# Performance work log

Measured on AMD Instinct MI355X. Metric: run time of the kernel, lower is better.

## Reference

```python
import jax, jax.numpy as jnp
import numpy as np


def setup_inputs() -> dict:
    key = jax.random.key(0)
    ks = jax.random.split(key, 7)
    B, N, D, A = 32, 128, 512, 512
    sD = 1.0 / np.sqrt(D)
    sA = 1.0 / np.sqrt(A)
    return {
        "x": jax.random.normal(ks[0], (B, N, D), dtype=jnp.float32),
        "W1": jax.random.normal(ks[1], (A, D), dtype=jnp.float32) * sD,
        "b1": jax.random.normal(ks[2], (A,), dtype=jnp.float32) * sD,
        "W2": jax.random.normal(ks[3], (A, D), dtype=jnp.float32) * sD,
        "b2": jax.random.normal(ks[4], (A,), dtype=jnp.float32) * sD,
        "Wout": jax.random.normal(ks[5], (A,), dtype=jnp.float32) * sA,
        "bout": jax.random.normal(ks[6], (1,), dtype=jnp.float32) * sA,
    }


def reference(x, W1, b1, W2, b2, Wout, bout):
    # x: (B, N, D)
    x1 = jnp.einsum('bnd,ad->bna', x, W1) + b1  # mlp1 -> (B, N, A)
    x2 = jnp.einsum('bnd,ad->bna', x, W2) + b2  # mlp2 -> (B, N, A)
    # outer broadcast add: x1.unsqueeze(1) + x2.unsqueeze(2) -> (B, N, N, A)
    s = x1[:, None, :, :] + x2[:, :, None, :]
    # include_root=False: drop ROOT row along dim 1 -> (B, N-1, N, A)
    s = s[:, 1:, :, :]
    s = jnp.tanh(s)
    # out linear A -> 1, then squeeze -> (B, N-1, N)
    return jnp.einsum('bija,a->bij', s, Wout) + bout[0]
```

## Files before the change

kernel.cpp:

```cpp
#include <hip/hip_runtime.h>
#include <hip/hip_bf16.h>

#define B_ 32
#define N_ 128
#define D_ 512
#define A_ 512
#define R_ (B_*N_)
#define OC 1024
#define CEXP 2.8853900817779268f

typedef __attribute__((ext_vector_type(8)))  short frag_ab;
typedef __attribute__((ext_vector_type(16))) float frag_c;

__device__ inline unsigned pack2bf(float a, float b) {
    unsigned ua = __builtin_bit_cast(unsigned, a) + 0x8000u;
    unsigned ub = __builtin_bit_cast(unsigned, b) + 0x8000u;
    return __builtin_amdgcn_perm(ub, ua, 0x07060302);
}
__device__ inline float bf2f_lo(unsigned u){ return __builtin_bit_cast(float, u << 16); }
__device__ inline float bf2f_hi(unsigned u){ return __builtin_bit_cast(float, u & 0xffff0000u); }
__device__ inline void wr8(float* dst, uint4 v) {
    *(float4*)dst     = float4{bf2f_lo(v.x),bf2f_hi(v.x),bf2f_lo(v.y),bf2f_hi(v.y)};
    *(float4*)(dst+4) = float4{bf2f_lo(v.z),bf2f_hi(v.z),bf2f_lo(v.w),bf2f_hi(v.w)};
}

__global__ __launch_bounds__(256) void k0_cvt(
    const float* __restrict__ X, const float* __restrict__ W1,
    const float* __restrict__ W2,
    unsigned short* __restrict__ Xb, unsigned short* __restrict__ W1b,
    unsigned short* __restrict__ W2b)
{
    const int NX = R_*D_/8, NW = A_*D_/8;
    int i = blockIdx.x*256 + threadIdx.x;
    const float* src; unsigned short* dst; int off;
    if (i < NX)            { src = X;  dst = Xb;  off = i; }
    else if (i < NX+NW)    { src = W1; dst = W1b; off = i-NX; }
    else if (i < NX+2*NW)  { src = W2; dst = W2b; off = i-NX-NW; }
    else return;
    float4 a = ((const float4*)src)[off*2];
    float4 c = ((const float4*)src)[off*2+1];
    uint4 o;
    o.x = pack2bf(a.x,a.y); o.y = pack2bf(a.z,a.w);
    o.z = pack2bf(c.x,c.y); o.w = pack2bf(c.z,c.w);
    ((uint4*)dst)[off] = o;
}

#define LDK1 36

__global__ __launch_bounds__(256) void k1_mfma(
    const unsigned short* __restrict__ Xb,
    const unsigned short* __restrict__ W1b, const float* __restrict__ b1,
    const unsigned short* __restrict__ W2b, const float* __restrict__ b2,
    unsigned short* __restrict__ Yb)
{
    __shared__ unsigned short As[2][128*LDK1];
    __shared__ unsigned short Bs[2][128*LDK1];

    const int t = threadIdx.x, lane = t&63, wid = t>>6;
    const int wr = wid>>1, wc = wid&1;
    const int row0 = blockIdx.x*128, col0 = blockIdx.y*128;
    const unsigned short* Wb = (col0 < A_) ? W1b : W2b;
    const float* bb = (col0 < A_) ? b1 : b2;
    const int wrow0 = col0 & (A_-1);

    const int srow = t>>1;
    const int scol = (t&1)*16;

    frag_c acc[2][2];
#pragma unroll
    for (int i=0;i<2;++i)
#pragma unroll
        for (int j=0;j<2;++j)
#pragma unroll
            for (int r=0;r<16;++r) acc[i][j][r] = 0.f;

    const int fr = lane & 31;
    const int ko = (lane >> 5) * 8;

    {
        const unsigned short* px = &Xb[(size_t)(row0 +srow)*D_ + scol];
        const unsigned short* pw = &Wb[(size_t)(wrow0+srow)*D_ + scol];
        uint4 a0 = *(const uint4*)px, a1 = *(const uint4*)(px+8);
        uint4 b0 = *(const uint4*)pw, b1v = *(const uint4*)(pw+8);
        *(uint4*)&As[0][srow*LDK1 + scol]     = a0;
        *(uint4*)&As[0][srow*LDK1 + scol + 8] = a1;
        *(uint4*)&Bs[0][srow*LDK1 + scol]     = b0;
        *(uint4*)&Bs[0][srow*LDK1 + scol + 8] = b1v;
    }
    __syncthreads();

#pragma unroll
    for (int s = 0; s < 16; ++s) {
        const int cur = s & 1;
        uint4 a0, a1, b0, b1v;
        if (s < 15) {
            const int k0 = (s+1)*32;
            const unsigned short* px = &Xb[(size_t)(row0 +srow)*D_ + k0 + scol];
            const unsigned short* pw = &Wb[(size_t)(wrow0+srow)*D_ + k0 + scol];
            a0 = *(const uint4*)px; a1 = *(const uint4*)(px+8);
            b0 = *(const uint4*)pw; b1v = *(const uint4*)(pw+8);
        }
        frag_ab af[2][2], bf[2][2];
#pragma unroll
        for (int mt=0; mt<2; ++mt)
#pragma unroll
            for (int ks=0; ks<2; ++ks) {
                af[mt][ks] = *(const frag_ab*)&As[cur][(wr*64+mt*32+fr)*LDK1 + ks*16 + ko];
                bf[mt][ks] = *(const frag_ab*)&Bs[cur][(wc*64+mt*32+fr)*LDK1 + ks*16 + ko];
            }
#pragma unroll
        for (int ks=0; ks<2; ++ks)
#pragma unroll
            for (int mt=0; mt<2; ++mt)
#pragma unroll
                for (int nt=0; nt<2; ++nt)
                    acc[mt][nt] = __builtin_amdgcn_mfma_f32_32x32x16_bf16(
                        af[mt][ks], bf[nt][ks], acc[mt][nt], 0, 0, 0);
        if (s < 15) {
            *(uint4*)&As[cur^1][srow*LDK1 + scol]     = a0;
            *(uint4*)&As[cur^1][srow*LDK1 + scol + 8] = a1;
            *(uint4*)&Bs[cur^1][srow*LDK1 + scol]     = b0;
            *(uint4*)&Bs[cur^1][srow*LDK1 + scol + 8] = b1v;
        }
        __syncthreads();
    }

#pragma unroll
    for (int mt=0; mt<2; ++mt) {
        const int rbase = row0 + wr*64 + mt*32 + 4*(lane>>5);
#pragma unroll
        for (int nt=0; nt<2; ++nt) {
            const int cc = col0 + wc*64 + nt*32 + (lane&31);
            const float bias = bb[cc & (A_-1)];
#pragma unroll
            for (int r=0; r<16; ++r) {
                const int rr = rbase + (r&3) + 8*(r>>2);
                float e = __builtin_amdgcn_exp2f(CEXP*(acc[mt][nt][r] + bias));
                Yb[(size_t)rr*OC + cc] =
                    (unsigned short)((__builtin_bit_cast(unsigned, e) + 0x8000u) >> 16);
            }
        }
    }
}

#define ACH2 128
#define LD2 (ACH2+4)

__global__ __launch_bounds__(256) void k2_tanh(
    const unsigned short* __restrict__ Yb,
    const float* __restrict__ Wout, const float* __restrict__ bout,
    float* __restrict__ out)
{
    __shared__ float e1s[32][LD2];
    __shared__ float e2s[32][LD2];
    __shared__ float wo[256];
    __shared__ float wsum_s[4];

    const int t  = threadIdx.x;
    const int jt = blockIdx.x, it = blockIdx.y;
    const int b  = blockIdx.z >> 1, ah = blockIdx.z & 1;
    const int abase = ah << 8;

    {
        float w = Wout[abase + t];
        wo[t] = w;
#pragma unroll
        for (int off=32; off>=1; off>>=1) w += __shfl_down(w, off, 64);
        if ((t&63)==0) wsum_s[t>>6] = w;
    }

    const unsigned short* yb = Yb + (size_t)b*N_*OC;
    const int sr = t>>4, sc = (t&15)*8;
    int i2a = it*32 + sr + 1;  if (i2a > 127) i2a = 127;
    int i2b = it*32 + sr + 17; if (i2b > 127) i2b = 127;
    const size_t o1a = (size_t)(jt*32+sr   )*OC + abase + sc;
    const size_t o1b = (size_t)(jt*32+sr+16)*OC + abase + sc;
    const size_t o2a = (size_t)i2a*OC + A_ + abase + sc;
    const size_t o2b = (size_t)i2b*OC + A_ + abase + sc;

    {
        uint4 v1a = *(const uint4*)&yb[o1a];
        uint4 v1b = *(const uint4*)&yb[o1b];
        uint4 v2a = *(const uint4*)&yb[o2a];
        uint4 v2b = *(const uint4*)&yb[o2b];
        wr8(&e1s[sr][sc], v1a); wr8(&e1s[sr+16][sc], v1b);
        wr8(&e2s[sr][sc], v2a); wr8(&e2s[sr+16][sc], v2b);
    }
    __syncthreads();

    uint4 n1a = *(const uint4*)&yb[o1a + ACH2];
    uint4 n1b = *(const uint4*)&yb[o1b + ACH2];
    uint4 n2a = *(const uint4*)&yb[o2a + ACH2];
    uint4 n2b = *(const uint4*)&yb[o2b + ACH2];

    const int jl = t&15, il = t>>4;
    float a00=0.f, a01=0.f, a10=0.f, a11=0.f;

#pragma unroll 4
    for (int c=0; c<ACH2; c+=2) {
        float2 u0 = *(const float2*)&e1s[jl   ][c];
        float2 u1 = *(const float2*)&e1s[jl+16][c];
        float2 v0 = *(const float2*)&e2s[il   ][c];
        float2 v1 = *(const float2*)&e2s[il+16][c];
        float2 w  = *(const float2*)&wo[c];
        { float r=fmaf(u0.x,v0.x,1.f), s=fmaf(u0.y,v0.y,1.f);
          a00 = fmaf(fmaf(w.x,s,w.y*r), __builtin_amdgcn_rcpf(r*s), a00); }
        { float r=fmaf(u1.x,v0.x,1.f), s=fmaf(u1.y,v0.y,1.f);
          a01 = fmaf(fmaf(w.x,s,w.y*r), __builtin_amdgcn_rcpf(r*s), a01); }
        { float r=fmaf(u0.x,v1.x,1.f), s=fmaf(u0.y,v1.y,1.f);
          a10 = fmaf(fmaf(w.x,s,w.y*r), __builtin_amdgcn_rcpf(r*s), a10); }
        { float r=fmaf(u1.x,v1.x,1.f), s=fmaf(u1.y,v1.y,1.f);
          a11 = fmaf(fmaf(w.x,s,w.y*r), __builtin_amdgcn_rcpf(r*s), a11); }
    }
    __syncthreads();
    wr8(&e1s[sr][sc], n1a); wr8(&e1s[sr+16][sc], n1b);
    wr8(&e2s[sr][sc], n2a); wr8(&e2s[sr+16][sc], n2b);
    __syncthreads();

#pragma unroll 4
    for (int c=0; c<ACH2; c+=2) {
        float2 u0 = *(const float2*)&e1s[jl   ][c];
        float2 u1 = *(const float2*)&e1s[jl+16][c];
        float2 v0 = *(const float2*)&e2s[il   ][c];
        float2 v1 = *(const float2*)&e2s[il+16][c];
        float2 w  = *(const float2*)&wo[ACH2 + c];
        { float r=fmaf(u0.x,v0.x,1.f), s=fmaf(u0.y,v0.y,1.f);
          a00 = fmaf(fmaf(w.x,s,w.y*r), __builtin_amdgcn_rcpf(r*s), a00); }
        { float r=fmaf(u1.x,v0.x,1.f), s=fmaf(u1.y,v0.y,1.f);
          a01 = fmaf(fmaf(w.x,s,w.y*r), __builtin_amdgcn_rcpf(r*s), a01); }
        { float r=fmaf(u0.x,v1.x,1.f), s=fmaf(u0.y,v1.y,1.f);
          a10 = fmaf(fmaf(w.x,s,w.y*r), __builtin_amdgcn_rcpf(r*s), a10); }
        { float r=fmaf(u1.x,v1.x,1.f), s=fmaf(u1.y,v1.y,1.f);
          a11 = fmaf(fmaf(w.x,s,w.y*r), __builtin_amdgcn_rcpf(r*s), a11); }
    }

    const float wsum = wsum_s[0]+wsum_s[1]+wsum_s[2]+wsum_s[3];
    const float base = wsum + (ah ? 0.f : bout[0]);
    const int i0 = it*32 + il, j0 = jt*32 + jl;
    float* ob = out + (size_t)b*127*128;
    if (i0 < 127) {
        atomicAdd(&ob[i0*128 + j0     ], base - 2.f*a00);
        atomicAdd(&ob[i0*128 + j0 + 16], base - 2.f*a01);
    }
    if (i0 + 16 < 127) {
        atomicAdd(&ob[(i0+16)*128 + j0     ], base - 2.f*a10);
        atomicAdd(&ob[(i0+16)*128 + j0 + 16], base - 2.f*a11);
    }
}

extern "C" void kernel_launch(void* const* d_in, const int* in_sizes, int n_in,
                              void* d_out, int out_size, void* d_ws, size_t ws_size,
                              hipStream_t stream) {
    const float* x    = (const float*)d_in[0];
    const float* W1   = (const float*)d_in[1];
    const float* b1   = (const float*)d_in[2];
    const float* W2   = (const float*)d_in[3];
    const float* b2   = (const float*)d_in[4];
    const float* Wout = (const float*)d_in[5];
    const float* bout = (const float*)d_in[6];
    float* out = (float*)d_out;

    char* ws = (char*)d_ws;
    unsigned short* Yb  = (unsigned short*)ws;
    unsigned short* Xb  = (unsigned short*)(ws + (8u<<20));
    unsigned short* W1b = (unsigned short*)(ws + (12u<<20));
    unsigned short* W2b = (unsigned short*)(ws + (12u<<20) + (1u<<19));

    k0_cvt<<<1280, 256, 0, stream>>>(x, W1, W2, Xb, W1b, W2b);

    dim3 g1(R_/128, OC/128);
    k1_mfma<<<g1, 256, 0, stream>>>(Xb, W1b, b1, W2b, b2, Yb);

    hipMemsetAsync(d_out, 0, (size_t)out_size*sizeof(float), stream);

    dim3 g2(4, 4, 2*B_);
    k2_tanh<<<g2, 256, 0, stream>>>(Yb, Wout, bout, out);
}
```

Measured before the change: 114.5 us.

## Use 4x4 register tiles with swizzled LDS in tanh-reduction kernel

Restructures the pairwise tanh kernel so each thread computes a 4x4 block of (i,j) outputs over a 64x64 tile, instead of 2x2 over 32x32. The A dimension is now split into four 128-wide chunks across grid.y, each loaded once rather than double-buffered. LDS rows use an XOR swizzle so the float4 reads of strided rows avoid bank conflicts. This cuts LDS traffic per FLOP through more register reuse, but raises register pressure, uses more LDS per block, and issues more atomics per output since four A-chunks now add into each element.

```diff
diff --git a/kernel.cpp b/kernel.cpp
--- a/kernel.cpp
+++ b/kernel.cpp
@@ -19,10 +19,6 @@
 }
 __device__ inline float bf2f_lo(unsigned u){ return __builtin_bit_cast(float, u << 16); }
 __device__ inline float bf2f_hi(unsigned u){ return __builtin_bit_cast(float, u & 0xffff0000u); }
-__device__ inline void wr8(float* dst, uint4 v) {
-    *(float4*)dst     = float4{bf2f_lo(v.x),bf2f_hi(v.x),bf2f_lo(v.y),bf2f_hi(v.y)};
-    *(float4*)(dst+4) = float4{bf2f_lo(v.z),bf2f_hi(v.z),bf2f_lo(v.w),bf2f_hi(v.w)};
-}
 
 __global__ __launch_bounds__(256) void k0_cvt(
     const float* __restrict__ X, const float* __restrict__ W1,
@@ -143,108 +139,95 @@
     }
 }
 
-#define ACH2 128
-#define LD2 (ACH2+4)
+#define LDW 132
+
+__device__ inline int swz(int r, int c) { return r*LDW + (c ^ (((r>>2)&7)<<2)); }
 
 __global__ __launch_bounds__(256) void k2_tanh(
     const unsigned short* __restrict__ Yb,
     const float* __restrict__ Wout, const float* __restrict__ bout,
     float* __restrict__ out)
 {
-    __shared__ float e1s[32][LD2];
-    __shared__ float e2s[32][LD2];
-    __shared__ float wo[256];
+    __shared__ float e1s[64*LDW];
+    __shared__ float e2s[64*LDW];
+    __shared__ float wo[128];
     __shared__ float wsum_s[4];
 
     const int t  = threadIdx.x;
-    const int jt = blockIdx.x, it = blockIdx.y;
-    const int b  = blockIdx.z >> 1, ah = blockIdx.z & 1;
-    const int abase = ah << 8;
+    const int jt = blockIdx.x & 1;
+    const int it = blockIdx.x >> 1;
+    const int ah = blockIdx.y;
+    const int b  = blockIdx.z;
+    const int abase = ah << 7;
 
     {
-        float w = Wout[abase + t];
-        wo[t] = w;
+        float w = (t < 128) ? Wout[abase + t] : 0.f;
+        if (t < 128) wo[t] = w;
 #pragma unroll
         for (int off=32; off>=1; off>>=1) w += __shfl_down(w, off, 64);
         if ((t&63)==0) wsum_s[t>>6] = w;
     }
 
     const unsigned short* yb = Yb + (size_t)b*N_*OC;
-    const int sr = t>>4, sc = (t&15)*8;
-    int i2a = it*32 + sr + 1;  if (i2a > 127) i2a = 127;
-    int i2b = it*32 + sr + 17; if (i2b > 127) i2b = 127;
-    const size_t o1a = (size_t)(jt*32+sr   )*OC + abase + sc;
-    const size_t o1b = (size_t)(jt*32+sr+16)*OC + abase + sc;
-    const size_t o2a = (size_t)i2a*OC + A_ + abase + sc;
-    const size_t o2b = (size_t)i2b*OC + A_ + abase + sc;
-
-    {
-        uint4 v1a = *(const uint4*)&yb[o1a];
-        uint4 v1b = *(const uint4*)&yb[o1b];
-        uint4 v2a = *(const uint4*)&yb[o2a];
-        uint4 v2b = *(const uint4*)&yb[o2b];
-        wr8(&e1s[sr][sc], v1a); wr8(&e1s[sr+16][sc], v1b);
-        wr8(&e2s[sr][sc], v2a); wr8(&e2s[sr+16][sc], v2b);
+    const int sr = t>>4;
+    const int sc = (t&15)*8;
+
+#pragma unroll
+    for (int q=0; q<4; ++q) {
+        const int r = q*16 + sr;
+        uint4 v1 = *(const uint4*)&yb[(size_t)(jt*64 + r)*OC + abase + sc];
+        int i2 = it*64 + r + 1; if (i2 > 127) i2 = 127;
+        uint4 v2 = *(const uint4*)&yb[(size_t)i2*OC + A_ + abase + sc];
+        *(float4*)&e1s[swz(r, sc)]   = float4{bf2f_lo(v1.x),bf2f_hi(v1.x),bf2f_lo(v1.y),bf2f_hi(v1.y)};
+        *(float4*)&e1s[swz(r, sc+4)] = float4{bf2f_lo(v1.z),bf2f_hi(v1.z),bf2f_lo(v1.w),bf2f_hi(v1.w)};
+        *(float4*)&e2s[swz(r, sc)]   = float4{bf2f_lo(v2.x),bf2f_hi(v2.x),bf2f_lo(v2.y),bf2f_hi(v2.y)};
+        *(float4*)&e2s[swz(r, sc+4)] = float4{bf2f_lo(v2.z),bf2f_hi(v2.z),bf2f_lo(v2.w),bf2f_hi(v2.w)};
     }
     __syncthreads();
 
-    uint4 n1a = *(const uint4*)&yb[o1a + ACH2];
-    uint4 n1b = *(const uint4*)&yb[o1b + ACH2];
-    uint4 n2a = *(const uint4*)&yb[o2a + ACH2];
-    uint4 n2b = *(const uint4*)&yb[o2b + ACH2];
-
     const int jl = t&15, il = t>>4;
-    float a00=0.f, a01=0.f, a10=0.f, a11=0.f;
-
-#pragma unroll 4
-    for (int c=0; c<ACH2; c+=2) {
-        float2 u0 = *(const float2*)&e1s[jl   ][c];
-        float2 u1 = *(const float2*)&e1s[jl+16][c];
-        float2 v0 = *(const float2*)&e2s[il   ][c];
-        float2 v1 = *(const float2*)&e2s[il+16][c];
-        float2 w  = *(const float2*)&wo[c];
-        { float r=fmaf(u0.x,v0.x,1.f), s=fmaf(u0.y,v0.y,1.f);
-          a00 = fmaf(fmaf(w.x,s,w.y*r), __builtin_amdgcn_rcpf(r*s), a00); }
-        { float r=fmaf(u1.x,v0.x,1.f), s=fmaf(u1.y,v0.y,1.f);
-          a01 = fmaf(fmaf(w.x,s,w.y*r), __builtin_amdgcn_rcpf(r*s), a01); }
-        { float r=fmaf(u0.x,v1.x,1.f), s=fmaf(u0.y,v1.y,1.f);
-          a10 = fmaf(fmaf(w.x,s,w.y*r), __builtin_amdgcn_rcpf(r*s), a10); }
-        { float r=fmaf(u1.x,v1.x,1.f), s=fmaf(u1.y,v1.y,1.f);
-          a11 = fmaf(fmaf(w.x,s,w.y*r), __builtin_amdgcn_rcpf(r*s), a11); }
-    }
-    __syncthreads();
-    wr8(&e1s[sr][sc], n1a); wr8(&e1s[sr+16][sc], n1b);
-    wr8(&e2s[sr][sc], n2a); wr8(&e2s[sr+16][sc], n2b);
-    __syncthreads();
-
-#pragma unroll 4
-    for (int c=0; c<ACH2; c+=2) {
-        float2 u0 = *(const float2*)&e1s[jl   ][c];
-        float2 u1 = *(const float2*)&e1s[jl+16][c];
-        float2 v0 = *(const float2*)&e2s[il   ][c];
-        float2 v1 = *(const float2*)&e2s[il+16][c];
-        float2 w  = *(const float2*)&wo[ACH2 + c];
-        { float r=fmaf(u0.x,v0.x,1.f), s=fmaf(u0.y,v0.y,1.f);
-          a00 = fmaf(fmaf(w.x,s,w.y*r), __builtin_amdgcn_rcpf(r*s), a00); }
-        { float r=fmaf(u1.x,v0.x,1.f), s=fmaf(u1.y,v0.y,1.f);
-          a01 = fmaf(fmaf(w.x,s,w.y*r), __builtin_amdgcn_rcpf(r*s), a01); }
-        { float r=fmaf(u0.x,v1.x,1.f), s=fmaf(u0.y,v1.y,1.f);
-          a10 = fmaf(fmaf(w.x,s,w.y*r), __builtin_amdgcn_rcpf(r*s), a10); }
-        { float r=fmaf(u1.x,v1.x,1.f), s=fmaf(u1.y,v1.y,1.f);
-          a11 = fmaf(fmaf(w.x,s,w.y*r), __builtin_amdgcn_rcpf(r*s), a11); }
+    float acc[4][4];
+#pragma unroll
+    for (int kj=0;kj<4;++kj)
+#pragma unroll
+        for (int ki=0;ki<4;++ki) acc[kj][ki] = 0.f;
+
+#pragma unroll 1
+    for (int c=0; c<128; c+=4) {
+        float4 u[4], v[4];
+#pragma unroll
+        for (int kj=0;kj<4;++kj) u[kj] = *(const float4*)&e1s[swz(4*jl+kj, c)];
+#pragma unroll
+        for (int ki=0;ki<4;++ki) v[ki] = *(const float4*)&e2s[swz(4*il+ki, c)];
+        float4 w4 = *(const float4*)&wo[c];
+#pragma unroll
+        for (int kj=0;kj<4;++kj)
+#pragma unroll
+            for (int ki=0;ki<4;++ki) {
+                float r0 = fmaf(u[kj].x, v[ki].x, 1.f);
+                float s0 = fmaf(u[kj].y, v[ki].y, 1.f);
+                acc[kj][ki] = fmaf(fmaf(w4.x, s0, w4.y*r0),
+                                   __builtin_amdgcn_rcpf(r0*s0), acc[kj][ki]);
+                float r1 = fmaf(u[kj].z, v[ki].z, 1.f);
+                float s1 = fmaf(u[kj].w, v[ki].w, 1.f);
+                acc[kj][ki] = fmaf(fmaf(w4.z, s1, w4.w*r1),
+                                   __builtin_amdgcn_rcpf(r1*s1), acc[kj][ki]);
+            }
     }
 
     const float wsum = wsum_s[0]+wsum_s[1]+wsum_s[2]+wsum_s[3];
     const float base = wsum + (ah ? 0.f : bout[0]);
-    const int i0 = it*32 + il, j0 = jt*32 + jl;
     float* ob = out + (size_t)b*127*128;
-    if (i0 < 127) {
-        atomicAdd(&ob[i0*128 + j0     ], base - 2.f*a00);
-        atomicAdd(&ob[i0*128 + j0 + 16], base - 2.f*a01);
-    }
-    if (i0 + 16 < 127) {
-        atomicAdd(&ob[(i0+16)*128 + j0     ], base - 2.f*a10);
-        atomicAdd(&ob[(i0+16)*128 + j0 + 16], base - 2.f*a11);
+#pragma unroll
+    for (int ki=0;ki<4;++ki) {
+        const int i0 = it*64 + 4*il + ki;
+        if (i0 < 127) {
+#pragma unroll
+            for (int kj=0;kj<4;++kj) {
+                const int j0 = jt*64 + 4*jl + kj;
+                atomicAdd(&ob[i0*128 + j0], base - 2.f*acc[kj][ki]);
+            }
+        }
     }
 }
 
@@ -273,6 +256,6 @@
 
     hipMemsetAsync(d_out, 0, (size_t)out_size*sizeof(float), stream);
 
-    dim3 g2(4, 4, 2*B_);
+    dim3 g2(4, 4, B_);
     k2_tanh<<<g2, 256, 0, stream>>>(Yb, Wout, bout, out);
 }
```

After: 131.8 us. +15.0%, slower.
